# Kernel tuning notes

Hardware: AMD Instinct MI355X
Metric: run time of the kernel (lower is better)

Reference implementation:

```python
import jax, jax.numpy as jnp
import numpy as np

ANCHORS = np.array([[10,13],[16,30],[33,23],[30,61],[62,45],[59,119],[116,90],[156,198],[373,326]], np.float32)
SCALES = np.array([8.0, 16.0, 32.0], np.float32)
SIZES = np.array([[76,76],[38,38],[19,19]], np.int64)
NUM_BOXES = 3
NUM_CLASSES = 80
NOOBJ_THR = 0.5
L_COORD, L_CLS, L_OBJ, L_NOOBJ = 1.0, 1.0, 1.0, 0.5

def _grid_constants():
    grids, anchs, scls = [], [], []
    for fi in range(3):
        w, h = int(SIZES[fi, 0]), int(SIZES[fi, 1])
        idx = np.arange(w * h * NUM_BOXES)
        cx = idx // (h * NUM_BOXES)          # matches torch: idx // (h*num_boxes)
        cy = (idx // NUM_BOXES) % h
        grids.append(np.stack([cx, cy], 1).astype(np.float32))
        anchs.append(np.tile(ANCHORS[fi * 3:(fi + 1) * 3], (w * h, 1)))
        scls.append(np.full(w * h * NUM_BOXES, SCALES[fi], np.float32))
    return (jnp.asarray(np.concatenate(grids)), jnp.asarray(np.concatenate(anchs)), jnp.asarray(np.concatenate(scls)))

GRID_CXY, ANCH_REP, SCALE_VEC = _grid_constants()  # [P,2],[P,2],[P]
STARTS = jnp.asarray(np.concatenate([[0], np.cumsum(SIZES.prod(1) * NUM_BOXES)[:-1]]).astype(np.int32))
ANCH_J = jnp.asarray(ANCHORS)
SCALES_J = jnp.asarray(SCALES)
SIZES_J = jnp.asarray(SIZES.astype(np.int32))

def _bce(p, t):
    # torch F.binary_cross_entropy clamps log terms at -100
    return -(t * jnp.clip(jnp.log(p), -100.0) + (1.0 - t) * jnp.clip(jnp.log1p(-p), -100.0))

def _box_iou_cxywh(b1, b2):
    c1, wh1 = b1[:, :2], b1[:, 2:4]
    c2, wh2 = b2[:, :2], b2[:, 2:4]
    lt = jnp.maximum(c1[:, None] - wh1[:, None] * 0.5, c2[None] - wh2[None] * 0.5)
    rb = jnp.minimum(c1[:, None] + wh1[:, None] * 0.5, c2[None] + wh2[None] * 0.5)
    wh = jnp.clip(rb - lt, 0.0)
    inter = wh[..., 0] * wh[..., 1]
    a1 = wh1[:, 0] * wh1[:, 1]
    a2 = wh2[:, 0] * wh2[:, 1]
    return inter / (a1[:, None] + a2[None] - inter)

def _per_image(predicts, pred_boxes, pred_obj, tboxes, tlabels, tscores):
    # predicts [P,85], pred_boxes [P,4] cxywh, pred_obj [P], tboxes [N,4] cxywh
    twh = tboxes[:, 2:4]
    inter = jnp.minimum(twh[:, None, 0], ANCH_J[None, :, 0]) * jnp.minimum(twh[:, None, 1], ANCH_J[None, :, 1])
    a_t = twh[:, 0] * twh[:, 1]
    a_a = ANCH_J[:, 0] * ANCH_J[:, 1]
    wh_ious = inter / (a_t[:, None] + a_a[None] - inter)        # vectorized wh_iou
    a_idx = jnp.argmax(wh_ious, axis=1)                          # [N]
    b_idx = (a_idx % NUM_BOXES).astype(jnp.int32)
    fi = a_idx // NUM_BOXES
    m_anch = ANCH_J[a_idx]
    scale_t = SCALES_J[fi]
    size_t = SIZES_J[fi]
    scaled = tboxes[:, :2] / scale_t[:, None]
    frac = scaled - jnp.floor(scaled)
    frac = jnp.where(frac == 0.0, 1.0, frac)                     # gt_txy[gt_txy==0]=1.0
    tl = (scaled - frac).astype(jnp.int32)
    gt_twh = jnp.log(twh / m_anch)
    gt_txywh = jnp.concatenate([frac, gt_twh], axis=1)
    pos_idx = STARTS[fi] + (tl[:, 0] * size_t[:, 1] + tl[:, 1]) * NUM_BOXES + b_idx
    pos = predicts[pos_idx]                                      # [N,85] gather
    pred_txywh = jnp.concatenate([jax.nn.sigmoid(pos[:, :2]), pos[:, 2:4]], axis=1)
    w = 2.0 - gt_twh[:, 0:1] * gt_twh[:, 1:2]
    lbox = jnp.mean(w * (pred_txywh - gt_txywh) ** 2)
    lbox = jnp.where(jnp.isinf(lbox), 0.0, lbox)
    lobj = jnp.mean(_bce(jax.nn.sigmoid(pos[:, 4]), tscores))
    gt_cls = jax.nn.one_hot(tlabels, NUM_CLASSES, dtype=pos.dtype)
    lcls = jnp.mean(_bce(jax.nn.sigmoid(pos[:, 5:]), gt_cls))
    max_iou = _box_iou_cxywh(pred_boxes, tboxes).max(axis=1)     # [P]
    pos_mask = jnp.zeros(predicts.shape[0], bool).at[pos_idx].set(True)
    no_mask = (max_iou < NOOBJ_THR) & (~pos_mask)
    neg_bce = -jnp.clip(jnp.log1p(-pred_obj), -100.0)            # BCE(p, 0)
    lnoobj = jnp.sum(jnp.where(no_mask, neg_bce, 0.0)) / jnp.maximum(jnp.sum(no_mask), 1).astype(neg_bce.dtype)
    return lbox, lobj, lcls, lnoobj

def _forward(feat0, feat1, feat2, target_boxes, target_labels, target_scores):
    B = feat0.shape[0]
    nf = feat0.shape[-1]
    predicts = jnp.concatenate([f.reshape(B, -1, nf) for f in (feat0, feat1, feat2)], axis=1)  # [B,P,85]
    pred_cxy = (GRID_CXY[None] + jax.nn.sigmoid(predicts[..., :2])) * SCALE_VEC[None, :, None]
    pred_wh = ANCH_REP[None] * jnp.exp(predicts[..., 2:4])
    pred_boxes = jnp.concatenate([pred_cxy, pred_wh], axis=-1)
    pred_obj = jax.nn.sigmoid(predicts[..., 4])
    lbox, lobj, lcls, lnoobj = jax.vmap(_per_image)(predicts, pred_boxes, pred_obj, target_boxes, target_labels, target_scores)
    return jnp.stack([L_COORD * lbox.mean(), L_CLS * lcls.mean(), L_OBJ * lobj.mean(), L_NOOBJ * lnoobj.mean()])

def setup_inputs() -> dict:
    key = jax.random.key(0)
    ks = jax.random.split(key, 6)
    B, N = 16, 20
    feat0 = jax.random.normal(ks[0], (B, 76, 76, 3, 85), jnp.float32)
    feat1 = jax.random.normal(ks[1], (B, 38, 38, 3, 85), jnp.float32)
    feat2 = jax.random.normal(ks[2], (B, 19, 19, 3, 85), jnp.float32)
    cxy = jax.random.uniform(ks[3], (B, N, 2), jnp.float32) * 500.0 + 50.0
    wh = jax.random.uniform(ks[4], (B, N, 2), jnp.float32) * 100.0 + 10.0
    target_boxes = jnp.concatenate([cxy, wh], axis=-1)
    target_labels = jax.random.randint(ks[5], (B, N), 0, 80)
    target_scores = jnp.ones((B, N), jnp.float32)
    return {"feat0": feat0, "feat1": feat1, "feat2": feat2, "target_boxes": target_boxes, "target_labels": target_labels, "target_scores": target_scores}

def reference(feat0, feat1, feat2, target_boxes, target_labels, target_scores):
    # returns [lbox, lcls, lobj, lnoobj] (lambda-weighted, batch-averaged)
    return _forward(feat0, feat1, feat2, target_boxes, target_labels, target_scores)
```

## Files before the change

### kernel.cpp

```cpp
#include <hip/hip_runtime.h>
#include <math.h>

#define NPRED 22743
#define NB 16
#define NT 20
#define NBLK2 45
#define NTBLK 5

__device__ __constant__ float c_anch[9][2] = {
    {10.f,13.f},{16.f,30.f},{33.f,23.f},{30.f,61.f},{62.f,45.f},
    {59.f,119.f},{116.f,90.f},{156.f,198.f},{373.f,326.f}};

__device__ __forceinline__ float sigm(float x){ return 1.0f/(1.0f+expf(-x)); }

__device__ __forceinline__ const float* row_base(const float* f0, const float* f1,
                                                 const float* f2, int b, int j){
    if (j < 17328) return f0 + ((size_t)b*17328 + j)*85;
    if (j < 21660) return f1 + ((size_t)b*4332  + (j-17328))*85;
    return f2 + ((size_t)b*1083 + (j-21660))*85;
}

__device__ __forceinline__ void row_geom(int j, float& scale, int& cx, int& cy, int& aidx){
    int local, fi;
    if (j < 17328){      local = j;        scale = 8.f;  cx = local/228; cy = (local/3)%76; fi = 0; }
    else if (j < 21660){ local = j-17328;  scale = 16.f; cx = local/114; cy = (local/3)%38; fi = 1; }
    else {               local = j-21660;  scale = 32.f; cx = local/57;  cy = (local/3)%19; fi = 2; }
    aidx = fi*3 + local%3;
}

__device__ __forceinline__ int best_anchor(float tw, float th){
    const float at = tw*th;
    int best = 0; float bi = -1.f;
    #pragma unroll
    for (int a = 0; a < 9; ++a){
        float aw = c_anch[a][0], ah = c_anch[a][1];
        float inter = fminf(tw,aw)*fminf(th,ah);
        float iou = inter/(at + aw*ah - inter);
        if (iou > bi){ bi = iou; best = a; }
    }
    return best;
}

__device__ __forceinline__ int pos_index(float cx, float cy, float tw, float th){
    const int best = best_anchor(tw,th);
    const int fi = best/3, bidx = best%3;
    const float scale = (fi==0)?8.f:((fi==1)?16.f:32.f);
    const int   hh    = (fi==0)?76 :((fi==1)?38 :19);
    const int   start = (fi==0)?0  :((fi==1)?17328:21660);
    float sx = cx/scale, sy = cy/scale;
    float fx = sx - floorf(sx); if (fx == 0.f) fx = 1.f;
    float fy = sy - floorf(sy); if (fy == 0.f) fy = 1.f;
    const int tlx = (int)(sx - fx);
    const int tly = (int)(sy - fy);
    return start + (tlx*hh + tly)*3 + bidx;
}

__device__ __forceinline__ void target_decode(float cx, float cy, float tw, float th,
                                              int& pidx, float& fx, float& fy,
                                              float& gtw, float& gth){
    const int best = best_anchor(tw,th);
    const int fi = best/3, bidx = best%3;
    const float scale = (fi==0)?8.f:((fi==1)?16.f:32.f);
    const int   hh    = (fi==0)?76 :((fi==1)?38 :19);
    const int   start = (fi==0)?0  :((fi==1)?17328:21660);
    const float aw = c_anch[best][0], ah = c_anch[best][1];
    float sx = cx/scale, sy = cy/scale;
    fx = sx - floorf(sx); if (fx == 0.f) fx = 1.f;
    fy = sy - floorf(sy); if (fy == 0.f) fy = 1.f;
    const int tlx = (int)(sx - fx);
    const int tly = (int)(sy - fy);
    gtw = logf(tw/aw); gth = logf(th/ah);
    pidx = start + (tlx*hh + tly)*3 + bidx;
}

__device__ __forceinline__ void noobj_row(int j, const float r[5],
                                          const float4* stb4, const int* spi,
                                          float& nb, int& cnt){
    float scale; int cx, cy, aidx;
    row_geom(j, scale, cx, cy, aidx);
    const float aw = c_anch[aidx][0], ah = c_anch[aidx][1];
    const float pcx = ((float)cx + sigm(r[0]))*scale;
    const float pcy = ((float)cy + sigm(r[1]))*scale;
    const float pw = aw*expf(r[2]);
    const float ph = ah*expf(r[3]);
    const float a1 = pw*ph;
    float maxiou = -INFINITY;
    #pragma unroll
    for (int t = 0; t < NT; ++t){
        float4 T = stb4[t];
        float ltx = fmaxf(pcx - pw*0.5f, T.x - T.z*0.5f);
        float lty = fmaxf(pcy - ph*0.5f, T.y - T.w*0.5f);
        float rbx = fminf(pcx + pw*0.5f, T.x + T.z*0.5f);
        float rby = fminf(pcy + ph*0.5f, T.y + T.w*0.5f);
        float iw = fmaxf(rbx - ltx, 0.f);
        float ih = fmaxf(rby - lty, 0.f);
        float inter = iw*ih;
        float iou = inter/(a1 + T.z*T.w - inter);
        maxiou = fmaxf(maxiou, iou);
    }
    bool pos = false;
    #pragma unroll
    for (int t = 0; t < NT; ++t) pos = pos || (spi[t] == j);
    if (maxiou < 0.5f && !pos){
        nb += fminf(log1pf(expf(r[4])), 100.f);
        cnt += 1;
    }
}

__global__ __launch_bounds__(256) void yolo_fused(
        const float* __restrict__ f0, const float* __restrict__ f1,
        const float* __restrict__ f2,
        const float* __restrict__ tb, const int* __restrict__ tlab,
        const float* __restrict__ tsc,
        float* __restrict__ part_s, int* __restrict__ part_c,
        float* __restrict__ pbox, float* __restrict__ pobj,
        float* __restrict__ pcls){
    const int b   = blockIdx.y;
    const int x   = blockIdx.x;
    const int tid = threadIdx.x;

    if (x < NBLK2){
        __shared__ float4 stb4[NT];
        __shared__ int    spi[NT];
        if (tid < NT) stb4[tid] = ((const float4*)tb)[b*NT + tid];
        if (tid >= 96 && tid < 96+NT){
            float4 box = ((const float4*)tb)[b*NT + (tid-96)];
            spi[tid-96] = pos_index(box.x, box.y, box.z, box.w);
        }
        __syncthreads();

        const int j0 = x*512 + tid;
        const int j1 = j0 + 256;
        const bool a0 = (j0 < NPRED), a1 = (j1 < NPRED);
        const float* P0 = row_base(f0,f1,f2,b, a0 ? j0 : 0);
        const float* P1 = row_base(f0,f1,f2,b, a1 ? j1 : 0);
        float r0[5], r1[5];
        #pragma unroll
        for (int k = 0; k < 5; ++k) r0[k] = P0[k];
        #pragma unroll
        for (int k = 0; k < 5; ++k) r1[k] = P1[k];

        float nb = 0.f; int cnt = 0;
        if (a0) noobj_row(j0, r0, stb4, spi, nb, cnt);
        if (a1) noobj_row(j1, r1, stb4, spi, nb, cnt);

        #pragma unroll
        for (int off = 32; off > 0; off >>= 1){
            nb  += __shfl_down(nb, off);
            cnt += __shfl_down(cnt, off);
        }
        __shared__ float ws_s[4];
        __shared__ int   ws_c[4];
        const int wid = tid >> 6;
        if ((tid & 63) == 0){ ws_s[wid] = nb; ws_c[wid] = cnt; }
        __syncthreads();
        if (tid == 0){
            part_s[b*NBLK2 + x] = ws_s[0]+ws_s[1]+ws_s[2]+ws_s[3];
            part_c[b*NBLK2 + x] = ws_c[0]+ws_c[1]+ws_c[2]+ws_c[3];
        }
    } else {
        const int w    = tid >> 6;
        const int lane = tid & 63;
        const int t    = (x - NBLK2)*4 + w;
        float4 box = ((const float4*)tb)[b*NT + t];
        int pidx; float fx, fy, gtw, gth;
        target_decode(box.x, box.y, box.z, box.w, pidx, fx, fy, gtw, gth);
        const float* p = row_base(f0,f1,f2,b,pidx);
        const int lab = tlab[b*NT + t];
        float s;
        {
            float pc = sigm(p[5+lane]);
            float lg  = fmaxf(logf(pc),    -100.f);
            float lg1 = fmaxf(log1pf(-pc), -100.f);
            float tt = (lane == lab) ? 1.f : 0.f;
            s = -(tt*lg + (1.f-tt)*lg1);
        }
        if (lane < 16){
            int c = 64 + lane;
            float pc = sigm(p[5+c]);
            float lg  = fmaxf(logf(pc),    -100.f);
            float lg1 = fmaxf(log1pf(-pc), -100.f);
            float tt = (c == lab) ? 1.f : 0.f;
            s += -(tt*lg + (1.f-tt)*lg1);
        }
        #pragma unroll
        for (int off = 32; off > 0; off >>= 1) s += __shfl_down(s, off);
        if (lane == 0){
            const float w2 = 2.f - gtw*gth;
            float d0 = sigm(p[0]) - fx;
            float d1 = sigm(p[1]) - fy;
            float d2 = p[2] - gtw;
            float d3 = p[3] - gth;
            pbox[b*NT + t] = w2*(d0*d0 + d1*d1 + d2*d2 + d3*d3);
            float po = sigm(p[4]);
            float ts = tsc[b*NT + t];
            float lg  = fmaxf(logf(po),    -100.f);
            float lg1 = fmaxf(log1pf(-po), -100.f);
            pobj[b*NT + t] = -(ts*lg + (1.f-ts)*lg1);
            pcls[b*NT + t] = s;
        }
    }
}

__global__ __launch_bounds__(256) void yolo_final(
        const float* __restrict__ part_s, const int* __restrict__ part_c,
        const float* __restrict__ pbox, const float* __restrict__ pobj,
        const float* __restrict__ pcls, float* __restrict__ out){
    const int tid  = threadIdx.x;
    const int w    = tid >> 6;
    const int lane = tid & 63;
    __shared__ float rb[NB], ro[NB], rc[NB], rn[NB];
    for (int b = w; b < NB; b += 4){
        float s = 0.f; int c = 0;
        if (lane < NBLK2){ s = part_s[b*NBLK2 + lane]; c = part_c[b*NBLK2 + lane]; }
        float A = 0.f, O = 0.f, C = 0.f;
        if (lane < NT){ A = pbox[b*NT + lane]; O = pobj[b*NT + lane]; C = pcls[b*NT + lane]; }
        #pragma unroll
        for (int off = 32; off > 0; off >>= 1){
            s += __shfl_down(s, off);
            c += __shfl_down(c, off);
            A += __shfl_down(A, off);
            O += __shfl_down(O, off);
            C += __shfl_down(C, off);
        }
        if (lane == 0){
            float lb = A/(float)(NT*4);
            if (isinf(lb)) lb = 0.f;
            rb[b] = lb;
            ro[b] = O/(float)NT;
            rc[b] = C/(float)(NT*80);
            rn[b] = s/(float)(c > 1 ? c : 1);
        }
    }
    __syncthreads();
    if (tid == 0){
        float sb=0.f, so=0.f, sc=0.f, sn=0.f;
        for (int b = 0; b < NB; ++b){ sb += rb[b]; so += ro[b]; sc += rc[b]; sn += rn[b]; }
        out[0] = sb/(float)NB;
        out[1] = sc/(float)NB;
        out[2] = so/(float)NB;
        out[3] = 0.5f*sn/(float)NB;
    }
}

extern "C" void kernel_launch(void* const* d_in, const int* in_sizes, int n_in,
                              void* d_out, int out_size, void* d_ws, size_t ws_size,
                              hipStream_t stream) {
    const float* f0  = (const float*)d_in[0];
    const float* f1  = (const float*)d_in[1];
    const float* f2  = (const float*)d_in[2];
    const float* tb  = (const float*)d_in[3];
    const int*   tlab= (const int*)  d_in[4];
    const float* tsc = (const float*)d_in[5];
    float* out = (float*)d_out;

    char* ws = (char*)d_ws;
    float* part_s = (float*)ws;
    int*   part_c = (int*)  (ws + 2880);
    float* pbox   = (float*)(ws + 5760);
    float* pobj   = (float*)(ws + 7040);
    float* pcls   = (float*)(ws + 8320);

    dim3 grid(NBLK2 + NTBLK, NB);
    yolo_fused<<<grid, 256, 0, stream>>>(f0, f1, f2, tb, tlab, tsc,
                                         part_s, part_c, pbox, pobj, pcls);
    yolo_final<<<1, 256, 0, stream>>>(part_s, part_c, pbox, pobj, pcls, out);
}
```

Baseline: 27.63 us.

## Replace per-row positive check with target-side correction and division-free IoU test

The per-row noobj test now compares 3*inter against union area instead of dividing to get IoU. Target rectangles and areas are precomputed once in shared memory. The 20-way positive-index comparison per row is dropped; target blocks instead recompute the qualifying test for their own positive row, deduplicate via a ballot, and emit corrections that the final kernel subtracts. Rows are also split one per thread across twice as many blocks, with float4 loads. This trades per-row work for extra target-side logic and a changed grid shape.

```diff
diff --git a/kernel.cpp b/kernel.cpp
--- a/kernel.cpp
+++ b/kernel.cpp
@@ -4,8 +4,9 @@
 #define NPRED 22743
 #define NB 16
 #define NT 20
-#define NBLK2 45
-#define NTBLK 5
+#define RBLK 89
+#define TBLK 5
+#define XTOT (RBLK + TBLK)
 
 __device__ __constant__ float c_anch[9][2] = {
     {10.f,13.f},{16.f,30.f},{33.f,23.f},{30.f,61.f},{62.f,45.f},
@@ -73,77 +74,70 @@
     pidx = start + (tlx*hh + tly)*3 + bidx;
 }
 
-__device__ __forceinline__ void noobj_row(int j, const float r[5],
-                                          const float4* stb4, const int* spi,
-                                          float& nb, int& cnt){
+__device__ __forceinline__ bool row_test(int j, float4 r4, float p4,
+                                         const float4* srect, const float* sa2,
+                                         float& sp){
     float scale; int cx, cy, aidx;
     row_geom(j, scale, cx, cy, aidx);
     const float aw = c_anch[aidx][0], ah = c_anch[aidx][1];
-    const float pcx = ((float)cx + sigm(r[0]))*scale;
-    const float pcy = ((float)cy + sigm(r[1]))*scale;
-    const float pw = aw*expf(r[2]);
-    const float ph = ah*expf(r[3]);
+    const float pcx = ((float)cx + sigm(r4.x))*scale;
+    const float pcy = ((float)cy + sigm(r4.y))*scale;
+    const float pw = aw*expf(r4.z);
+    const float ph = ah*expf(r4.w);
     const float a1 = pw*ph;
-    float maxiou = -INFINITY;
+    const float pxl = pcx - pw*0.5f, pyl = pcy - ph*0.5f;
+    const float pxr = pcx + pw*0.5f, pyr = pcy + ph*0.5f;
+    float md = -1.f;
     #pragma unroll
     for (int t = 0; t < NT; ++t){
-        float4 T = stb4[t];
-        float ltx = fmaxf(pcx - pw*0.5f, T.x - T.z*0.5f);
-        float lty = fmaxf(pcy - ph*0.5f, T.y - T.w*0.5f);
-        float rbx = fminf(pcx + pw*0.5f, T.x + T.z*0.5f);
-        float rby = fminf(pcy + ph*0.5f, T.y + T.w*0.5f);
-        float iw = fmaxf(rbx - ltx, 0.f);
-        float ih = fmaxf(rby - lty, 0.f);
+        float4 T = srect[t];
+        float iw = fmaxf(fminf(pxr, T.z) - fmaxf(pxl, T.x), 0.f);
+        float ih = fmaxf(fminf(pyr, T.w) - fmaxf(pyl, T.y), 0.f);
         float inter = iw*ih;
-        float iou = inter/(a1 + T.z*T.w - inter);
-        maxiou = fmaxf(maxiou, iou);
-    }
-    bool pos = false;
-    #pragma unroll
-    for (int t = 0; t < NT; ++t) pos = pos || (spi[t] == j);
-    if (maxiou < 0.5f && !pos){
-        nb += fminf(log1pf(expf(r[4])), 100.f);
-        cnt += 1;
-    }
-}
-
-__global__ __launch_bounds__(256) void yolo_fused(
+        md = fmaxf(md, fmaf(3.f, inter, -(a1 + sa2[t])));
+    }
+    sp = fminf(log1pf(expf(p4)), 100.f);
+    return md < 0.f;
+}
+
+__global__ __launch_bounds__(256) void yolo_main(
         const float* __restrict__ f0, const float* __restrict__ f1,
         const float* __restrict__ f2,
         const float* __restrict__ tb, const int* __restrict__ tlab,
         const float* __restrict__ tsc,
         float* __restrict__ part_s, int* __restrict__ part_c,
         float* __restrict__ pbox, float* __restrict__ pobj,
-        float* __restrict__ pcls){
+        float* __restrict__ pcls,
+        float* __restrict__ corr_s, int* __restrict__ corr_c){
     const int b   = blockIdx.y;
     const int x   = blockIdx.x;
     const int tid = threadIdx.x;
 
-    if (x < NBLK2){
-        __shared__ float4 stb4[NT];
-        __shared__ int    spi[NT];
-        if (tid < NT) stb4[tid] = ((const float4*)tb)[b*NT + tid];
-        if (tid >= 96 && tid < 96+NT){
-            float4 box = ((const float4*)tb)[b*NT + (tid-96)];
-            spi[tid-96] = pos_index(box.x, box.y, box.z, box.w);
-        }
-        __syncthreads();
-
-        const int j0 = x*512 + tid;
-        const int j1 = j0 + 256;
-        const bool a0 = (j0 < NPRED), a1 = (j1 < NPRED);
-        const float* P0 = row_base(f0,f1,f2,b, a0 ? j0 : 0);
-        const float* P1 = row_base(f0,f1,f2,b, a1 ? j1 : 0);
-        float r0[5], r1[5];
-        #pragma unroll
-        for (int k = 0; k < 5; ++k) r0[k] = P0[k];
-        #pragma unroll
-        for (int k = 0; k < 5; ++k) r1[k] = P1[k];
+    __shared__ float4 sbox[NT];
+    __shared__ float4 srect[NT];
+    __shared__ float  sa2[NT];
+    if (tid < NT){
+        float4 T = ((const float4*)tb)[b*NT + tid];
+        sbox[tid]  = T;
+        srect[tid] = make_float4(T.x - T.z*0.5f, T.y - T.w*0.5f,
+                                 T.x + T.z*0.5f, T.y + T.w*0.5f);
+        sa2[tid] = T.z * T.w;
+    }
+    __syncthreads();
+
+    if (x < RBLK){
+        const int j = x*256 + tid;
+        const bool valid = (j < NPRED);
+        const float* P = row_base(f0,f1,f2,b, valid ? j : 0);
+        const float4 r4 = *reinterpret_cast<const float4*>(P);
+        const float  p4 = P[4];
 
         float nb = 0.f; int cnt = 0;
-        if (a0) noobj_row(j0, r0, stb4, spi, nb, cnt);
-        if (a1) noobj_row(j1, r1, stb4, spi, nb, cnt);
-
+        if (valid){
+            float sp;
+            bool qual = row_test(j, r4, p4, srect, sa2, sp);
+            if (qual){ nb = sp; cnt = 1; }
+        }
         #pragma unroll
         for (int off = 32; off > 0; off >>= 1){
             nb  += __shfl_down(nb, off);
@@ -155,17 +149,29 @@
         if ((tid & 63) == 0){ ws_s[wid] = nb; ws_c[wid] = cnt; }
         __syncthreads();
         if (tid == 0){
-            part_s[b*NBLK2 + x] = ws_s[0]+ws_s[1]+ws_s[2]+ws_s[3];
-            part_c[b*NBLK2 + x] = ws_c[0]+ws_c[1]+ws_c[2]+ws_c[3];
+            part_s[b*RBLK + x] = ws_s[0]+ws_s[1]+ws_s[2]+ws_s[3];
+            part_c[b*RBLK + x] = ws_c[0]+ws_c[1]+ws_c[2]+ws_c[3];
         }
     } else {
         const int w    = tid >> 6;
         const int lane = tid & 63;
-        const int t    = (x - NBLK2)*4 + w;
-        float4 box = ((const float4*)tb)[b*NT + t];
+        const int t    = (x - RBLK)*4 + w;
+
+        const int bl = (lane < NT) ? lane : (NT-1);
+        float4 BL = sbox[bl];
+        int pidx_l = pos_index(BL.x, BL.y, BL.z, BL.w);
+        float4 box = sbox[t];
         int pidx; float fx, fy, gtw, gth;
         target_decode(box.x, box.y, box.z, box.w, pidx, fx, fy, gtw, gth);
+        unsigned long long mask = __ballot(pidx_l == pidx);
+        const bool dup = (mask & ((1ull << t) - 1ull)) != 0ull;
+
         const float* p = row_base(f0,f1,f2,b,pidx);
+        const float4 r4 = *reinterpret_cast<const float4*>(p);
+        const float  p4 = p[4];
+        float sp;
+        bool qual = row_test(pidx, r4, p4, srect, sa2, sp);
+
         const int lab = tlab[b*NT + t];
         float s;
         {
@@ -185,19 +191,23 @@
         }
         #pragma unroll
         for (int off = 32; off > 0; off >>= 1) s += __shfl_down(s, off);
+
         if (lane == 0){
             const float w2 = 2.f - gtw*gth;
-            float d0 = sigm(p[0]) - fx;
-            float d1 = sigm(p[1]) - fy;
-            float d2 = p[2] - gtw;
-            float d3 = p[3] - gth;
+            float d0 = sigm(r4.x) - fx;
+            float d1 = sigm(r4.y) - fy;
+            float d2 = r4.z - gtw;
+            float d3 = r4.w - gth;
             pbox[b*NT + t] = w2*(d0*d0 + d1*d1 + d2*d2 + d3*d3);
-            float po = sigm(p[4]);
+            float po = sigm(p4);
             float ts = tsc[b*NT + t];
             float lg  = fmaxf(logf(po),    -100.f);
             float lg1 = fmaxf(log1pf(-po), -100.f);
             pobj[b*NT + t] = -(ts*lg + (1.f-ts)*lg1);
             pcls[b*NT + t] = s;
+            const bool take = qual && !dup;
+            corr_s[b*NT + t] = take ? sp : 0.f;
+            corr_c[b*NT + t] = take ? 1 : 0;
         }
     }
 }
@@ -205,23 +215,31 @@
 __global__ __launch_bounds__(256) void yolo_final(
         const float* __restrict__ part_s, const int* __restrict__ part_c,
         const float* __restrict__ pbox, const float* __restrict__ pobj,
-        const float* __restrict__ pcls, float* __restrict__ out){
+        const float* __restrict__ pcls,
+        const float* __restrict__ corr_s, const int* __restrict__ corr_c,
+        float* __restrict__ out){
     const int tid  = threadIdx.x;
     const int w    = tid >> 6;
     const int lane = tid & 63;
     __shared__ float rb[NB], ro[NB], rc[NB], rn[NB];
     for (int b = w; b < NB; b += 4){
         float s = 0.f; int c = 0;
-        if (lane < NBLK2){ s = part_s[b*NBLK2 + lane]; c = part_c[b*NBLK2 + lane]; }
-        float A = 0.f, O = 0.f, C = 0.f;
-        if (lane < NT){ A = pbox[b*NT + lane]; O = pobj[b*NT + lane]; C = pcls[b*NT + lane]; }
+        if (lane < RBLK){ s = part_s[b*RBLK + lane]; c = part_c[b*RBLK + lane]; }
+        if (lane + 64 < RBLK){ s += part_s[b*RBLK + lane + 64]; c += part_c[b*RBLK + lane + 64]; }
+        float A = 0.f, O = 0.f, C = 0.f, CS = 0.f; int CC = 0;
+        if (lane < NT){
+            A = pbox[b*NT + lane]; O = pobj[b*NT + lane]; C = pcls[b*NT + lane];
+            CS = corr_s[b*NT + lane]; CC = corr_c[b*NT + lane];
+        }
         #pragma unroll
         for (int off = 32; off > 0; off >>= 1){
-            s += __shfl_down(s, off);
-            c += __shfl_down(c, off);
-            A += __shfl_down(A, off);
-            O += __shfl_down(O, off);
-            C += __shfl_down(C, off);
+            s  += __shfl_down(s, off);
+            c  += __shfl_down(c, off);
+            A  += __shfl_down(A, off);
+            O  += __shfl_down(O, off);
+            C  += __shfl_down(C, off);
+            CS += __shfl_down(CS, off);
+            CC += __shfl_down(CC, off);
         }
         if (lane == 0){
             float lb = A/(float)(NT*4);
@@ -229,7 +247,9 @@
             rb[b] = lb;
             ro[b] = O/(float)NT;
             rc[b] = C/(float)(NT*80);
-            rn[b] = s/(float)(c > 1 ? c : 1);
+            int   cnt = c - CC;
+            float sum = s - CS;
+            rn[b] = sum/(float)(cnt > 1 ? cnt : 1);
         }
     }
     __syncthreads();
@@ -256,13 +276,17 @@
 
     char* ws = (char*)d_ws;
     float* part_s = (float*)ws;
-    int*   part_c = (int*)  (ws + 2880);
-    float* pbox   = (float*)(ws + 5760);
-    float* pobj   = (float*)(ws + 7040);
-    float* pcls   = (float*)(ws + 8320);
-
-    dim3 grid(NBLK2 + NTBLK, NB);
-    yolo_fused<<<grid, 256, 0, stream>>>(f0, f1, f2, tb, tlab, tsc,
-                                         part_s, part_c, pbox, pobj, pcls);
-    yolo_final<<<1, 256, 0, stream>>>(part_s, part_c, pbox, pobj, pcls, out);
-}
+    int*   part_c = (int*)  (ws + 5696);
+    float* pbox   = (float*)(ws + 11392);
+    float* pobj   = (float*)(ws + 12672);
+    float* pcls   = (float*)(ws + 13952);
+    float* corr_s = (float*)(ws + 15232);
+    int*   corr_c = (int*)  (ws + 16512);
+
+    dim3 grid(XTOT, NB);
+    yolo_main<<<grid, 256, 0, stream>>>(f0, f1, f2, tb, tlab, tsc,
+                                        part_s, part_c, pbox, pobj, pcls,
+                                        corr_s, corr_c);
+    yolo_final<<<1, 256, 0, stream>>>(part_s, part_c, pbox, pobj, pcls,
+                                      corr_s, corr_c, out);
+}
```

Result: slower. 29.71 us (+7.5%).
